# Optimization experiments

Hardware: AMD Instinct MI355X
Metric: run time of the kernel (lower is better)

The kernel has to match this reference:

```python
import jax, jax.numpy as jnp
import numpy as np

N_NODES = 50000
N_EDGES = 800000
MUL = 32                      # multiplicity of 0e and 1o in node_feats
AVG_NUM_NEIGHBORS = 16.0
INV_SQRT3 = 1.0 / np.sqrt(3.0)


def setup_inputs() -> dict:
    key = jax.random.key(0)
    ks = jax.random.split(key, 7)
    return {
        "node_feats": jax.random.normal(ks[0], (N_NODES, 4 * MUL), dtype=jnp.float32),
        "edge_attrs": jax.random.normal(ks[1], (N_EDGES, 4), dtype=jnp.float32),
        "senders": jax.random.randint(ks[2], (N_EDGES,), 0, N_NODES, dtype=jnp.int64) if jax.config.jax_enable_x64 else jax.random.randint(ks[2], (N_EDGES,), 0, N_NODES, dtype=jnp.int32),
        "receivers": jax.random.randint(ks[3], (N_EDGES,), 0, N_NODES, dtype=jnp.int32),
        "w_mlp0": jax.random.normal(ks[4], (1, 64), dtype=jnp.float32),
        "w_mlp1": jax.random.normal(ks[5], (64, 64), dtype=jnp.float32),
        "w_mlp2": jax.random.normal(ks[6], (64, 4 * MUL), dtype=jnp.float32),
    }


def reference(node_feats, edge_attrs, senders, receivers, w_mlp0, w_mlp1, w_mlp2):
    # node_feats layout: [N, MUL] scalars (0e) then [N, MUL*3] flattened vectors (1o)
    s = node_feats[:, :MUL]                          # [N, MUL]   32x0e
    v = node_feats[:, MUL:].reshape(-1, MUL, 3)      # [N, MUL,3] 32x1o

    # gather sender features per edge
    s_e = s[senders]                                 # [E, MUL]
    v_e = v[senders]                                 # [E, MUL, 3]

    ea0 = edge_attrs[:, :1]                          # [E,1]  1x0e
    ea1 = edge_attrs[:, 1:4]                         # [E,3]  1x1o

    # equivariant tensor product with edge_attrs.filter(drop='0e') = 1x1o,
    # keeping only target irreps (0e,1o):
    #   0e x 1o -> 1o : scalar * vector
    tp_1o = s_e[:, :, None] * ea1[:, None, :]        # [E, MUL, 3]
    #   1o x 1o -> 0e : dot / sqrt(3)  (component normalization)
    tp_0e = jnp.einsum('eci,ei->ec', v_e, ea1) * INV_SQRT3  # [E, MUL]

    # concatenate([msgs.filter(target), tp]).regroup() -> 64x0e + 64x1o
    scalars = jnp.concatenate([s_e, tp_0e], axis=1)          # [E, 2*MUL]
    vectors = jnp.concatenate([v_e, tp_1o], axis=1)          # [E, 2*MUL, 3]

    # MLP gate on scalar edge attrs (e3nn MLP: no bias, 1/sqrt(fan_in), swish)
    h = jax.nn.swish(ea0 @ w_mlp0 / jnp.sqrt(1.0))           # [E,64]
    h = jax.nn.swish(h @ w_mlp1 / jnp.sqrt(64.0))            # [E,64]
    mix = h @ w_mlp2 / jnp.sqrt(64.0)                        # [E, 4*MUL]

    n_sc = 2 * MUL
    scalars = scalars * mix[:, :n_sc]                        # gate 0e
    vectors = vectors * mix[:, n_sc:, None]                  # gate 1o (one scalar per vector)

    msgs = jnp.concatenate([scalars, vectors.reshape(vectors.shape[0], -1)], axis=1)  # [E, 8*MUL]

    # scatter-add messages to receivers
    out = jax.ops.segment_sum(msgs, receivers, num_segments=N_NODES)  # [N, 8*MUL]
    return out / jnp.sqrt(AVG_NUM_NEIGHBORS)
```

## Files before the change

### kernel.cpp

```cpp
#include <hip/hip_runtime.h>
#include <hip/hip_fp16.h>
#include <cstdint>

#define N_NODES   50000
#define FEAT      128
#define OUTF      256
#define MAX_EDGES 800000
#define CAP       64
#define INV_SQRT3 0.57735026918962576f
#define NW        (64 + 64*64 + 64*128)
#define TB_BLKS   ((N_NODES * 32 + 255) / 256)

__device__ float    g_wf[NW];
__device__ float    g_lut[65536 * 128];
__device__ uint16_t g_tbl[N_NODES * FEAT];
__device__ int      g_flags[4];
__device__ int      g_cnt[N_NODES];
__device__ uint4    g_ebuf[N_NODES * CAP];
__device__ unsigned char g_used[65536];

__device__ __forceinline__ float b2f(uint32_t b) {
    union { uint32_t u; float f; } v; v.u = b << 16; return v.f;
}
__device__ __forceinline__ uint32_t f2b_bits(float f) {
    union { float f; uint32_t u; } v; v.f = f;
    uint32_t u = v.u;
    u += 0x7fffu + ((u >> 16) & 1u);
    return u >> 16;
}
__device__ __forceinline__ float swishf(float x) {
    return x / (1.0f + __expf(-x));
}
__device__ __forceinline__ float sane(float x) {
    union { float f; uint32_t u; } v; v.f = x;
    return (((v.u >> 23) & 0xffu) >= 0x8Du) ? 0.0f : x;
}
__device__ __forceinline__ float loadf(const void* p, int i, int isbf) {
    return isbf ? b2f(((const uint16_t*)p)[i]) : ((const float*)p)[i];
}
__device__ __forceinline__ float h2f(uint32_t bits16) {
    return __half2float(__ushort_as_half((unsigned short)bits16));
}

__global__ __launch_bounds__(256) void init_kernel(
    const void* nf, const void* ea, const void* w0, const void* w1, const void* w2,
    const int* snd, const int* rcv, int snd_force64, int n_edges)
{
    int bx = blockIdx.x, t = threadIdx.x;
    if (bx == 0) {
        __shared__ int viol[4];
        if (t < 4) viol[t] = 0;
        __syncthreads();
        {
            int n = N_NODES * FEAT; int step = (n / 256) | 1;
            long long i = (long long)t * step;
            if (i < n) {
                uint32_t e = (((const uint16_t*)nf)[i] >> 7) & 0xffu;
                if (e > 140u) atomicOr(&viol[2], 1);
            }
        }
        {
            int n = n_edges * 4; int step = (n / 256) | 1;
            long long i = (long long)t * step;
            if (i < n) {
                uint32_t e = (((const uint16_t*)ea)[i] >> 7) & 0xffu;
                if (e > 140u) atomicOr(&viol[3], 1);
            }
        }
        if (t < 64) {
            int i = 2 * t + 1;
            if (i < 2 * n_edges) {
                if (snd[i] != 0) atomicOr(&viol[0], 1);
                if (rcv[i] != 0) atomicOr(&viol[1], 1);
            }
        }
        __syncthreads();
        if (t == 0) {
            g_flags[0] = snd_force64 ? 1 : !viol[0];
            g_flags[1] = !viol[1];
            g_flags[2] = !viol[2];
            g_flags[3] = !viol[3];
        }
    } else if (bx <= 196) {
        int i = (bx - 1) * 256 + t;
        if (i < N_NODES) g_cnt[i] = 0;
    } else if (bx <= 245) {
        __shared__ int wv[3];
        if (t < 3) wv[t] = 0;
        __syncthreads();
        if (t < 64) {
            uint32_t e = (((const uint16_t*)w0)[t] >> 7) & 0xffu;
            if (e > 140u) atomicOr(&wv[0], 1);
        }
        { int i = t * 17; if (i < 4096) {
            uint32_t e = (((const uint16_t*)w1)[i] >> 7) & 0xffu;
            if (e > 140u) atomicOr(&wv[1], 1); } }
        { int i = t * 33; if (i < 8192) {
            uint32_t e = (((const uint16_t*)w2)[i] >> 7) & 0xffu;
            if (e > 140u) atomicOr(&wv[2], 1); } }
        __syncthreads();
        int i = (bx - 197) * 256 + t;
        if (i < 64)             g_wf[i] = loadf(w0, i, !wv[0]);
        else if (i < 64 + 4096) g_wf[i] = loadf(w1, i - 64, !wv[1]);
        else if (i < NW)        g_wf[i] = loadf(w2, i - (64 + 4096), !wv[2]);
    } else {
        __shared__ int viol;
        if (t == 0) viol = 0;
        __syncthreads();
        {
            int n = n_edges * 4; int step = (n / 256) | 1;
            long long i = (long long)t * step;
            if (i < n) {
                uint32_t e = (((const uint16_t*)ea)[i] >> 7) & 0xffu;
                if (e > 140u) atomicOr(&viol, 1);
            }
        }
        __syncthreads();
        int f3l = !viol;
        int e = (bx - 246) * 256 + t;
        if (e < n_edges) {
            uint32_t b0 = f3l ? (uint32_t)((const uint16_t*)ea)[4 * e]
                              : f2b_bits(((const float*)ea)[4 * e]);
            g_used[b0 & 0xffffu] = 1;
        }
    }
}

__global__ __launch_bounds__(256) void prep_kernel(
    const void* __restrict__ nf, const void* __restrict__ ea,
    const int* __restrict__ snd, const int* __restrict__ rcv,
    int n_edges, int eb)
{
    int bx = blockIdx.x;
    if (bx < 1024) {
        int w = bx * 4 + (threadIdx.x >> 6);
        int lane = threadIdx.x & 63;
        int f = (lane < 16) ? (g_used[w * 16 + lane] != 0) : 0;
        unsigned long long mask = __ballot(f) & 0xffffull;
        if (!mask) return;
        const float* w1 = g_wf + 64;
        const float* w2 = g_wf + 64 + 4096;
        float w0l = g_wf[lane];
        while (mask) {
            int bit = __builtin_ctzll((unsigned long long)mask);
            mask &= mask - 1;
            int r = w * 16 + bit;
            float x = b2f((uint32_t)r);
            float h0 = swishf(x * w0l);
            float a = 0.f;
            #pragma unroll 8
            for (int k = 0; k < 64; ++k)
                a += __shfl(h0, k, 64) * w1[k * 64 + lane];
            float h1 = swishf(a * 0.125f);
            float a0 = 0.f, a1 = 0.f;
            #pragma unroll 8
            for (int k = 0; k < 64; ++k) {
                float h1k = __shfl(h1, k, 64);
                a0 += h1k * w2[k * 128 + lane];
                a1 += h1k * w2[k * 128 + 64 + lane];
            }
            float s1c = 0.125f * 0.25f;
            float s0c = (lane >= 32) ? s1c * INV_SQRT3 : s1c;
            float* dst = g_lut + (size_t)r * 128;
            int cc = lane & 31;
            if (lane < 32) {
                dst[cc * 4 + 0] = sane(a0 * s0c);
                dst[cc * 4 + 2] = sane(a1 * s1c);
            } else {
                dst[cc * 4 + 1] = sane(a0 * s0c);
                dst[cc * 4 + 3] = sane(a1 * s1c);
            }
        }
    } else if (bx < 1024 + eb) {
        int e = (bx - 1024) * 256 + threadIdx.x;
        if (e >= n_edges) return;
        int ri = g_flags[1] ? rcv[2 * e] : rcv[e];
        ri = min(max(ri, 0), N_NODES - 1);
        uint32_t b0; float ex, ey, ez;
        if (g_flags[3]) {
            uint2 w = ((const uint2*)ea)[e];
            b0 = w.x & 0xffffu;
            ex = b2f(w.x >> 16);
            ey = b2f(w.y & 0xffffu);
            ez = b2f(w.y >> 16);
        } else {
            float4 w = ((const float4*)ea)[e];
            b0 = f2b_bits(w.x) & 0xffffu;
            ex = w.y; ey = w.z; ez = w.w;
        }
        int s_ = g_flags[0] ? snd[2 * e] : snd[e];
        s_ = min(max(s_, 0), N_NODES - 1);
        uint4 pk;
        pk.x = ((uint32_t)s_ << 16) | b0;
        pk.y = __float_as_uint(ex);
        pk.z = __float_as_uint(ey);
        pk.w = __float_as_uint(ez);
        int p = atomicAdd(&g_cnt[ri], 1);
        if (p < CAP) g_ebuf[ri * CAP + p] = pk;
    } else {
        int i = (bx - 1024 - eb) * 256 + threadIdx.x;
        if (i < N_NODES * 32) {
            int node = i >> 5, c = i & 31;
            int f2 = g_flags[2];
            int rb = node * FEAT;
            float s  = loadf(nf, rb + c, f2);
            float v0 = loadf(nf, rb + 32 + 3 * c + 0, f2);
            float v1 = loadf(nf, rb + 32 + 3 * c + 1, f2);
            float v2 = loadf(nf, rb + 32 + 3 * c + 2, f2);
            uint32_t lo = (uint32_t)__half_as_ushort(__float2half(s))
                        | ((uint32_t)__half_as_ushort(__float2half(v0)) << 16);
            uint32_t hi = (uint32_t)__half_as_ushort(__float2half(v1))
                        | ((uint32_t)__half_as_ushort(__float2half(v2)) << 16);
            ((uint2*)g_tbl)[i] = make_uint2(lo, hi);
        }
    }
}

__global__ __launch_bounds__(256) void gather_kernel(void* __restrict__ out)
{
    int wid = (blockIdx.x * 256 + threadIdx.x) >> 6;
    int lane = threadIdx.x & 63;
    if (wid >= N_NODES) return;
    int c = lane & 31;
    int half = lane >> 5;
    const int f2 = g_flags[2];
    int deg = min(g_cnt[wid], CAP);

    float o0 = 0.f, o1 = 0.f, o2 = 0.f, o3 = 0.f,
          o4 = 0.f, o5 = 0.f, o6 = 0.f, o7 = 0.f;

    uint32_t pk_p = 0;
    float ex_p = 0.f, ey_p = 0.f, ez_p = 0.f;
    if (lane < deg) {
        uint4 w = g_ebuf[wid * CAP + lane];
        pk_p = w.x;
        ex_p = __uint_as_float(w.y);
        ey_p = __uint_as_float(w.z);
        ez_p = __uint_as_float(w.w);
    }

    const uint2* tbl = (const uint2*)g_tbl;

    for (int j = 0; j < deg; j += 4) {
        int jjA = j + half, jjB = j + 2 + half;
        float gA = (jjA < deg) ? 1.0f : 0.0f;
        float gB = (jjB < deg) ? 1.0f : 0.0f;
        int jxA = (jjA < deg) ? jjA : 0;
        int jxB = (jjB < deg) ? jjB : 0;

        uint32_t pkA = (uint32_t)__shfl((int)pk_p, jxA, 64);
        uint32_t pkB = (uint32_t)__shfl((int)pk_p, jxB, 64);
        float exA = __shfl(ex_p, jxA, 64), eyA = __shfl(ey_p, jxA, 64), ezA = __shfl(ez_p, jxA, 64);
        float exB = __shfl(ex_p, jxB, 64), eyB = __shfl(ey_p, jxB, 64), ezB = __shfl(ez_p, jxB, 64);

        const float4 mA = *(const float4*)(g_lut + (size_t)(pkA & 0xffffu) * 128 + c * 4);
        const float4 mB = *(const float4*)(g_lut + (size_t)(pkB & 0xffffu) * 128 + c * 4);
        uint2 hA = tbl[(size_t)(pkA >> 16) * 32 + c];
        uint2 hB = tbl[(size_t)(pkB >> 16) * 32 + c];

        float sA  = h2f(hA.x & 0xffffu), vA0 = h2f(hA.x >> 16);
        float vA1 = h2f(hA.y & 0xffffu), vA2 = h2f(hA.y >> 16);
        float sB  = h2f(hB.x & 0xffffu), vB0 = h2f(hB.x >> 16);
        float vB1 = h2f(hB.y & 0xffffu), vB2 = h2f(hB.y >> 16);

        {
            float m0 = mA.x * gA, m1 = mA.y * gA, m2 = mA.z * gA, m3 = mA.w * gA;
            o0 += sA * m0;
            o1 += (vA0 * exA + vA1 * eyA + vA2 * ezA) * m1;
            o2 += vA0 * m2; o3 += vA1 * m2; o4 += vA2 * m2;
            float sm3 = sA * m3;
            o5 += exA * sm3; o6 += eyA * sm3; o7 += ezA * sm3;
        }
        {
            float m0 = mB.x * gB, m1 = mB.y * gB, m2 = mB.z * gB, m3 = mB.w * gB;
            o0 += sB * m0;
            o1 += (vB0 * exB + vB1 * eyB + vB2 * ezB) * m1;
            o2 += vB0 * m2; o3 += vB1 * m2; o4 += vB2 * m2;
            float sm3 = sB * m3;
            o5 += exB * sm3; o6 += eyB * sm3; o7 += ezB * sm3;
        }
    }

    o0 += __shfl_xor(o0, 32, 64);
    o1 += __shfl_xor(o1, 32, 64);
    o2 += __shfl_xor(o2, 32, 64);
    o3 += __shfl_xor(o3, 32, 64);
    o4 += __shfl_xor(o4, 32, 64);
    o5 += __shfl_xor(o5, 32, 64);
    o6 += __shfl_xor(o6, 32, 64);
    o7 += __shfl_xor(o7, 32, 64);

    if (half == 0) {
        size_t bo = (size_t)wid * OUTF;
        if (f2) {
            uint16_t* o = (uint16_t*)out;
            o[bo + c]             = (uint16_t)f2b_bits(o0);
            o[bo + 32 + c]        = (uint16_t)f2b_bits(o1);
            o[bo + 64 + 3*c + 0]  = (uint16_t)f2b_bits(o2);
            o[bo + 64 + 3*c + 1]  = (uint16_t)f2b_bits(o3);
            o[bo + 64 + 3*c + 2]  = (uint16_t)f2b_bits(o4);
            o[bo + 160 + 3*c + 0] = (uint16_t)f2b_bits(o5);
            o[bo + 160 + 3*c + 1] = (uint16_t)f2b_bits(o6);
            o[bo + 160 + 3*c + 2] = (uint16_t)f2b_bits(o7);
        } else {
            float* o = (float*)out;
            o[bo + c]             = o0;
            o[bo + 32 + c]        = o1;
            o[bo + 64 + 3*c + 0]  = o2;
            o[bo + 64 + 3*c + 1]  = o3;
            o[bo + 64 + 3*c + 2]  = o4;
            o[bo + 160 + 3*c + 0] = o5;
            o[bo + 160 + 3*c + 1] = o6;
            o[bo + 160 + 3*c + 2] = o7;
        }
    }
}

extern "C" void kernel_launch(void* const* d_in, const int* in_sizes, int n_in,
                              void* d_out, int out_size, void* d_ws, size_t ws_size,
                              hipStream_t stream) {
    (void)n_in; (void)out_size; (void)d_ws; (void)ws_size;
    const void* nf = d_in[0];
    const void* ea = d_in[1];
    const int* snd = (const int*)d_in[2];
    const int* rcv = (const int*)d_in[3];
    const void* w0 = d_in[4];
    const void* w1 = d_in[5];
    const void* w2 = d_in[6];

    int n_edges = in_sizes[1] / 4;
    if (n_edges > MAX_EDGES) n_edges = MAX_EDGES;
    int snd_force64 = (in_sizes[2] == 2 * in_sizes[3]) ? 1 : 0;
    int eb = (n_edges + 255) / 256;

    init_kernel<<<246 + eb, 256, 0, stream>>>(nf, ea, w0, w1, w2, snd, rcv, snd_force64, n_edges);
    prep_kernel<<<1024 + eb + TB_BLKS, 256, 0, stream>>>(nf, ea, snd, rcv, n_edges, eb);
    gather_kernel<<<(N_NODES + 3) / 4, 256, 0, stream>>>(d_out);
}
```

Baseline: 258.0 us.

## Merge edge bucketing into init, halve LUT and slot storage, rebalance LUT build

Folds edge bucketing and the node-feature fp16 table build into the init kernel, so the middle kernel only evaluates the gate MLP. The gate LUT is stored as fp16 instead of fp32, and each per-receiver slot shrinks from 16 to 8 bytes by storing the edge index; gather then re-reads the edge vector directly. The LUT build assigns LUT rows to waves in a strided pattern to spread the used entries more evenly across waves. Receiver counters are now zeroed inside the gather kernel for the next call rather than in init. The trade-off is extra fp16 rounding of gate values and a dependence on the counters starting at zero on the first call.

```diff
diff --git a/kernel.cpp b/kernel.cpp
--- a/kernel.cpp
+++ b/kernel.cpp
@@ -12,11 +12,11 @@
 #define TB_BLKS   ((N_NODES * 32 + 255) / 256)
 
 __device__ float    g_wf[NW];
-__device__ float    g_lut[65536 * 128];
+__device__ uint16_t g_lut16[65536 * 128];
 __device__ uint16_t g_tbl[N_NODES * FEAT];
 __device__ int      g_flags[4];
 __device__ int      g_cnt[N_NODES];
-__device__ uint4    g_ebuf[N_NODES * CAP];
+__device__ uint2    g_slot[N_NODES * CAP];
 __device__ unsigned char g_used[65536];
 
 __device__ __forceinline__ float b2f(uint32_t b) {
@@ -40,6 +40,9 @@
 }
 __device__ __forceinline__ float h2f(uint32_t bits16) {
     return __half2float(__ushort_as_half((unsigned short)bits16));
+}
+__device__ __forceinline__ uint32_t f2h(float x) {
+    return (uint32_t)__half_as_ushort(__float2half(x));
 }
 
 __global__ __launch_bounds__(256) void init_kernel(
@@ -51,22 +54,18 @@
         __shared__ int viol[4];
         if (t < 4) viol[t] = 0;
         __syncthreads();
-        {
-            int n = N_NODES * FEAT; int step = (n / 256) | 1;
+        {   int n = N_NODES * FEAT; int step = (n / 256) | 1;
             long long i = (long long)t * step;
             if (i < n) {
                 uint32_t e = (((const uint16_t*)nf)[i] >> 7) & 0xffu;
                 if (e > 140u) atomicOr(&viol[2], 1);
-            }
-        }
-        {
-            int n = n_edges * 4; int step = (n / 256) | 1;
+            } }
+        {   int n = n_edges * 4; int step = (n / 256) | 1;
             long long i = (long long)t * step;
             if (i < n) {
                 uint32_t e = (((const uint16_t*)ea)[i] >> 7) & 0xffu;
                 if (e > 140u) atomicOr(&viol[3], 1);
-            }
-        }
+            } }
         if (t < 64) {
             int i = 2 * t + 1;
             if (i < 2 * n_edges) {
@@ -81,10 +80,7 @@
             g_flags[2] = !viol[2];
             g_flags[3] = !viol[3];
         }
-    } else if (bx <= 196) {
-        int i = (bx - 1) * 256 + t;
-        if (i < N_NODES) g_cnt[i] = 0;
-    } else if (bx <= 245) {
+    } else if (bx <= 49) {
         __shared__ int wv[3];
         if (t < 3) wv[t] = 0;
         __syncthreads();
@@ -99,132 +95,123 @@
             uint32_t e = (((const uint16_t*)w2)[i] >> 7) & 0xffu;
             if (e > 140u) atomicOr(&wv[2], 1); } }
         __syncthreads();
-        int i = (bx - 197) * 256 + t;
+        int i = (bx - 1) * 256 + t;
         if (i < 64)             g_wf[i] = loadf(w0, i, !wv[0]);
         else if (i < 64 + 4096) g_wf[i] = loadf(w1, i - 64, !wv[1]);
         else if (i < NW)        g_wf[i] = loadf(w2, i - (64 + 4096), !wv[2]);
-    } else {
-        __shared__ int viol;
-        if (t == 0) viol = 0;
-        __syncthreads();
-        {
-            int n = n_edges * 4; int step = (n / 256) | 1;
+    } else if (bx <= 49 + TB_BLKS) {
+        __shared__ int nv;
+        if (t == 0) nv = 0;
+        __syncthreads();
+        {   int n = N_NODES * FEAT; int step = (n / 256) | 1;
             long long i = (long long)t * step;
             if (i < n) {
-                uint32_t e = (((const uint16_t*)ea)[i] >> 7) & 0xffu;
-                if (e > 140u) atomicOr(&viol, 1);
+                uint32_t e = (((const uint16_t*)nf)[i] >> 7) & 0xffu;
+                if (e > 140u) atomicOr(&nv, 1);
+            } }
+        __syncthreads();
+        int f2l = !nv;
+        int i = (bx - 50) * 256 + t;
+        if (i < N_NODES * 32) {
+            int node = i >> 5, c = i & 31;
+            int rb = node * FEAT;
+            float s  = loadf(nf, rb + c, f2l);
+            float v0 = loadf(nf, rb + 32 + 3 * c + 0, f2l);
+            float v1 = loadf(nf, rb + 32 + 3 * c + 1, f2l);
+            float v2 = loadf(nf, rb + 32 + 3 * c + 2, f2l);
+            uint32_t lo = f2h(s)  | (f2h(v0) << 16);
+            uint32_t hi = f2h(v1) | (f2h(v2) << 16);
+            ((uint2*)g_tbl)[i] = make_uint2(lo, hi);
+        }
+    } else {
+        __shared__ int ev[3];
+        if (t < 3) ev[t] = 0;
+        __syncthreads();
+        {   int n = n_edges * 4; int step = (n / 256) | 1;
+            long long i = (long long)t * step;
+            if (i < n) {
+                uint32_t x = (((const uint16_t*)ea)[i] >> 7) & 0xffu;
+                if (x > 140u) atomicOr(&ev[2], 1);
+            } }
+        if (t < 64) {
+            int i = 2 * t + 1;
+            if (i < 2 * n_edges) {
+                if (snd[i] != 0) atomicOr(&ev[0], 1);
+                if (rcv[i] != 0) atomicOr(&ev[1], 1);
             }
         }
         __syncthreads();
-        int f3l = !viol;
-        int e = (bx - 246) * 256 + t;
+        int f0l = snd_force64 ? 1 : !ev[0];
+        int f1l = !ev[1];
+        int f3l = !ev[2];
+        int e = (bx - 50 - TB_BLKS) * 256 + t;
         if (e < n_edges) {
+            int ri = f1l ? rcv[2 * e] : rcv[e];
+            ri = min(max(ri, 0), N_NODES - 1);
             uint32_t b0 = f3l ? (uint32_t)((const uint16_t*)ea)[4 * e]
                               : f2b_bits(((const float*)ea)[4 * e]);
-            g_used[b0 & 0xffffu] = 1;
-        }
-    }
-}
-
-__global__ __launch_bounds__(256) void prep_kernel(
-    const void* __restrict__ nf, const void* __restrict__ ea,
-    const int* __restrict__ snd, const int* __restrict__ rcv,
-    int n_edges, int eb)
-{
-    int bx = blockIdx.x;
-    if (bx < 1024) {
-        int w = bx * 4 + (threadIdx.x >> 6);
-        int lane = threadIdx.x & 63;
-        int f = (lane < 16) ? (g_used[w * 16 + lane] != 0) : 0;
-        unsigned long long mask = __ballot(f) & 0xffffull;
-        if (!mask) return;
-        const float* w1 = g_wf + 64;
-        const float* w2 = g_wf + 64 + 4096;
-        float w0l = g_wf[lane];
-        while (mask) {
-            int bit = __builtin_ctzll((unsigned long long)mask);
-            mask &= mask - 1;
-            int r = w * 16 + bit;
-            float x = b2f((uint32_t)r);
-            float h0 = swishf(x * w0l);
-            float a = 0.f;
-            #pragma unroll 8
-            for (int k = 0; k < 64; ++k)
-                a += __shfl(h0, k, 64) * w1[k * 64 + lane];
-            float h1 = swishf(a * 0.125f);
-            float a0 = 0.f, a1 = 0.f;
-            #pragma unroll 8
-            for (int k = 0; k < 64; ++k) {
-                float h1k = __shfl(h1, k, 64);
-                a0 += h1k * w2[k * 128 + lane];
-                a1 += h1k * w2[k * 128 + 64 + lane];
-            }
-            float s1c = 0.125f * 0.25f;
-            float s0c = (lane >= 32) ? s1c * INV_SQRT3 : s1c;
-            float* dst = g_lut + (size_t)r * 128;
-            int cc = lane & 31;
-            if (lane < 32) {
-                dst[cc * 4 + 0] = sane(a0 * s0c);
-                dst[cc * 4 + 2] = sane(a1 * s1c);
-            } else {
-                dst[cc * 4 + 1] = sane(a0 * s0c);
-                dst[cc * 4 + 3] = sane(a1 * s1c);
-            }
-        }
-    } else if (bx < 1024 + eb) {
-        int e = (bx - 1024) * 256 + threadIdx.x;
-        if (e >= n_edges) return;
-        int ri = g_flags[1] ? rcv[2 * e] : rcv[e];
-        ri = min(max(ri, 0), N_NODES - 1);
-        uint32_t b0; float ex, ey, ez;
-        if (g_flags[3]) {
-            uint2 w = ((const uint2*)ea)[e];
-            b0 = w.x & 0xffffu;
-            ex = b2f(w.x >> 16);
-            ey = b2f(w.y & 0xffffu);
-            ez = b2f(w.y >> 16);
-        } else {
-            float4 w = ((const float4*)ea)[e];
-            b0 = f2b_bits(w.x) & 0xffffu;
-            ex = w.y; ey = w.z; ez = w.w;
-        }
-        int s_ = g_flags[0] ? snd[2 * e] : snd[e];
-        s_ = min(max(s_, 0), N_NODES - 1);
-        uint4 pk;
-        pk.x = ((uint32_t)s_ << 16) | b0;
-        pk.y = __float_as_uint(ex);
-        pk.z = __float_as_uint(ey);
-        pk.w = __float_as_uint(ez);
-        int p = atomicAdd(&g_cnt[ri], 1);
-        if (p < CAP) g_ebuf[ri * CAP + p] = pk;
-    } else {
-        int i = (bx - 1024 - eb) * 256 + threadIdx.x;
-        if (i < N_NODES * 32) {
-            int node = i >> 5, c = i & 31;
-            int f2 = g_flags[2];
-            int rb = node * FEAT;
-            float s  = loadf(nf, rb + c, f2);
-            float v0 = loadf(nf, rb + 32 + 3 * c + 0, f2);
-            float v1 = loadf(nf, rb + 32 + 3 * c + 1, f2);
-            float v2 = loadf(nf, rb + 32 + 3 * c + 2, f2);
-            uint32_t lo = (uint32_t)__half_as_ushort(__float2half(s))
-                        | ((uint32_t)__half_as_ushort(__float2half(v0)) << 16);
-            uint32_t hi = (uint32_t)__half_as_ushort(__float2half(v1))
-                        | ((uint32_t)__half_as_ushort(__float2half(v2)) << 16);
-            ((uint2*)g_tbl)[i] = make_uint2(lo, hi);
-        }
-    }
-}
-
-__global__ __launch_bounds__(256) void gather_kernel(void* __restrict__ out)
+            b0 &= 0xffffu;
+            int s_ = f0l ? snd[2 * e] : snd[e];
+            s_ = min(max(s_, 0), N_NODES - 1);
+            g_used[b0] = 1;
+            int p = atomicAdd(&g_cnt[ri], 1);
+            if (p < CAP) g_slot[ri * CAP + p] = make_uint2(((uint32_t)s_ << 16) | b0, (uint32_t)e);
+        }
+    }
+}
+
+__global__ __launch_bounds__(256) void lut_kernel() {
+    int w = blockIdx.x * 4 + (threadIdx.x >> 6);
+    int lane = threadIdx.x & 63;
+    int f = (lane < 16) ? (g_used[w + lane * 4096] != 0) : 0;
+    unsigned long long mask = __ballot(f) & 0xffffull;
+    if (!mask) return;
+    const float* w1 = g_wf + 64;
+    const float* w2 = g_wf + 64 + 4096;
+    float w0l = g_wf[lane];
+    while (mask) {
+        int k = __builtin_ctzll(mask);
+        mask &= mask - 1;
+        int r = w + k * 4096;
+        float x = b2f((uint32_t)r);
+        float h0 = swishf(x * w0l);
+        float a = 0.f;
+        #pragma unroll 8
+        for (int kk = 0; kk < 64; ++kk)
+            a += __shfl(h0, kk, 64) * w1[kk * 64 + lane];
+        float h1 = swishf(a * 0.125f);
+        float a0 = 0.f, a1 = 0.f;
+        #pragma unroll 8
+        for (int kk = 0; kk < 64; ++kk) {
+            float h1k = __shfl(h1, kk, 64);
+            a0 += h1k * w2[kk * 128 + lane];
+            a1 += h1k * w2[kk * 128 + 64 + lane];
+        }
+        float s1c = 0.125f * 0.25f;
+        float s0c = (lane >= 32) ? s1c * INV_SQRT3 : s1c;
+        float pa = sane(a0 * s0c);
+        float pb = sane(a1 * s1c);
+        float qa = __shfl_xor(pa, 32, 64);
+        float qb = __shfl_xor(pb, 32, 64);
+        if (lane < 32) {
+            uint32_t lo = f2h(pa) | (f2h(qa) << 16);
+            uint32_t hi = f2h(pb) | (f2h(qb) << 16);
+            ((uint2*)(g_lut16 + (size_t)r * 128))[lane] = make_uint2(lo, hi);
+        }
+    }
+}
+
+__global__ __launch_bounds__(256) void gather_kernel(
+    const void* __restrict__ ea, void* __restrict__ out)
 {
     int wid = (blockIdx.x * 256 + threadIdx.x) >> 6;
     int lane = threadIdx.x & 63;
     if (wid >= N_NODES) return;
     int c = lane & 31;
     int half = lane >> 5;
-    const int f2 = g_flags[2];
+    const int f2 = g_flags[2], f3 = g_flags[3];
     int deg = min(g_cnt[wid], CAP);
+    if (lane == 0) g_cnt[wid] = 0;
 
     float o0 = 0.f, o1 = 0.f, o2 = 0.f, o3 = 0.f,
           o4 = 0.f, o5 = 0.f, o6 = 0.f, o7 = 0.f;
@@ -232,11 +219,18 @@
     uint32_t pk_p = 0;
     float ex_p = 0.f, ey_p = 0.f, ez_p = 0.f;
     if (lane < deg) {
-        uint4 w = g_ebuf[wid * CAP + lane];
-        pk_p = w.x;
-        ex_p = __uint_as_float(w.y);
-        ey_p = __uint_as_float(w.z);
-        ez_p = __uint_as_float(w.w);
+        uint2 sl = g_slot[wid * CAP + lane];
+        pk_p = sl.x;
+        int e = (int)sl.y;
+        if (f3) {
+            uint2 w = ((const uint2*)ea)[e];
+            ex_p = b2f(w.x >> 16);
+            ey_p = b2f(w.y & 0xffffu);
+            ez_p = b2f(w.y >> 16);
+        } else {
+            float4 w = ((const float4*)ea)[e];
+            ex_p = w.y; ey_p = w.z; ez_p = w.w;
+        }
     }
 
     const uint2* tbl = (const uint2*)g_tbl;
@@ -253,8 +247,8 @@
         float exA = __shfl(ex_p, jxA, 64), eyA = __shfl(ey_p, jxA, 64), ezA = __shfl(ez_p, jxA, 64);
         float exB = __shfl(ex_p, jxB, 64), eyB = __shfl(ey_p, jxB, 64), ezB = __shfl(ez_p, jxB, 64);
 
-        const float4 mA = *(const float4*)(g_lut + (size_t)(pkA & 0xffffu) * 128 + c * 4);
-        const float4 mB = *(const float4*)(g_lut + (size_t)(pkB & 0xffffu) * 128 + c * 4);
+        uint2 mAu = ((const uint2*)(g_lut16 + (size_t)(pkA & 0xffffu) * 128))[c];
+        uint2 mBu = ((const uint2*)(g_lut16 + (size_t)(pkB & 0xffffu) * 128))[c];
         uint2 hA = tbl[(size_t)(pkA >> 16) * 32 + c];
         uint2 hB = tbl[(size_t)(pkB >> 16) * 32 + c];
 
@@ -264,7 +258,8 @@
         float vB1 = h2f(hB.y & 0xffffu), vB2 = h2f(hB.y >> 16);
 
         {
-            float m0 = mA.x * gA, m1 = mA.y * gA, m2 = mA.z * gA, m3 = mA.w * gA;
+            float m0 = h2f(mAu.x & 0xffffu) * gA, m1 = h2f(mAu.x >> 16) * gA;
+            float m2 = h2f(mAu.y & 0xffffu) * gA, m3 = h2f(mAu.y >> 16) * gA;
             o0 += sA * m0;
             o1 += (vA0 * exA + vA1 * eyA + vA2 * ezA) * m1;
             o2 += vA0 * m2; o3 += vA1 * m2; o4 += vA2 * m2;
@@ -272,7 +267,8 @@
             o5 += exA * sm3; o6 += eyA * sm3; o7 += ezA * sm3;
         }
         {
-            float m0 = mB.x * gB, m1 = mB.y * gB, m2 = mB.z * gB, m3 = mB.w * gB;
+            float m0 = h2f(mBu.x & 0xffffu) * gB, m1 = h2f(mBu.x >> 16) * gB;
+            float m2 = h2f(mBu.y & 0xffffu) * gB, m3 = h2f(mBu.y >> 16) * gB;
             o0 += sB * m0;
             o1 += (vB0 * exB + vB1 * eyB + vB2 * ezB) * m1;
             o2 += vB0 * m2; o3 += vB1 * m2; o4 += vB2 * m2;
@@ -333,7 +329,7 @@
     int snd_force64 = (in_sizes[2] == 2 * in_sizes[3]) ? 1 : 0;
     int eb = (n_edges + 255) / 256;
 
-    init_kernel<<<246 + eb, 256, 0, stream>>>(nf, ea, w0, w1, w2, snd, rcv, snd_force64, n_edges);
-    prep_kernel<<<1024 + eb + TB_BLKS, 256, 0, stream>>>(nf, ea, snd, rcv, n_edges, eb);
-    gather_kernel<<<(N_NODES + 3) / 4, 256, 0, stream>>>(d_out);
-}
+    init_kernel<<<50 + TB_BLKS + eb, 256, 0, stream>>>(nf, ea, w0, w1, w2, snd, rcv, snd_force64, n_edges);
+    lut_kernel<<<1024, 256, 0, stream>>>();
+    gather_kernel<<<(N_NODES + 3) / 4, 256, 0, stream>>>(ea, d_out);
+}
```

Measured after the change: 215.2 us. 1.2x faster.
